# Performance work log

Hardware: AMD Instinct MI355X
Metric: run time of the kernel (lower is better)

The kernel has to match this reference:

```python
import jax, jax.numpy as jnp
import numpy as np

MAX_LENGTH = 10
SOS = 0
H = 1024
V = 32000
B = 256
S = 64


def setup_inputs() -> dict:
    key = jax.random.key(0)
    ks = jax.random.split(key, 16)
    sc = 1.0 / np.sqrt(H)
    return {
        "encoder_outputs": jax.random.normal(ks[0], (B, S, H), jnp.float32),
        "encoder_hidden": jax.random.normal(ks[1], (1, B, H), jnp.float32),
        "target_tensor": jax.random.randint(ks[2], (B, MAX_LENGTH), 0, V),
        "embedding": jax.random.normal(ks[3], (V, H), jnp.float32),
        "Wa_w": jax.random.uniform(ks[4], (H, H), jnp.float32, -sc, sc),
        "Wa_b": jax.random.uniform(ks[5], (H,), jnp.float32, -sc, sc),
        "Ua_w": jax.random.uniform(ks[6], (H, H), jnp.float32, -sc, sc),
        "Ua_b": jax.random.uniform(ks[7], (H,), jnp.float32, -sc, sc),
        "Va_w": jax.random.uniform(ks[8], (1, H), jnp.float32, -sc, sc),
        "Va_b": jax.random.uniform(ks[9], (1,), jnp.float32, -sc, sc),
        "gru_w_ih": jax.random.uniform(ks[10], (3 * H, 2 * H), jnp.float32, -sc, sc),
        "gru_w_hh": jax.random.uniform(ks[11], (3 * H, H), jnp.float32, -sc, sc),
        "gru_b_ih": jax.random.uniform(ks[12], (3 * H,), jnp.float32, -sc, sc),
        "gru_b_hh": jax.random.uniform(ks[13], (3 * H,), jnp.float32, -sc, sc),
        "out_w": jax.random.uniform(ks[14], (V, H), jnp.float32, -sc, sc),
        "out_b": jax.random.uniform(ks[15], (V,), jnp.float32, -sc, sc),
    }


def reference(encoder_outputs, encoder_hidden, target_tensor, embedding,
              Wa_w, Wa_b, Ua_w, Ua_b, Va_w, Va_b,
              gru_w_ih, gru_w_hh, gru_b_ih, gru_b_hh, out_w, out_b):
    keys = encoder_outputs                      # [B,S,H]
    # Ua(keys) is step-invariant: hoist out of the decode loop.
    Uk = jnp.einsum('bsh,kh->bsk', keys, Ua_w) + Ua_b  # [B,S,H]
    h0 = encoder_hidden[0]                      # [B,H]
    # teacher forcing: input at step i is SOS for i=0 else target[:, i-1]
    toks = jnp.concatenate(
        [jnp.full((B, 1), SOS, dtype=target_tensor.dtype),
         target_tensor[:, :MAX_LENGTH - 1]], axis=1).T  # [T,B]

    def step(h, tok):
        emb = embedding[tok]                               # [B,H] (dropout = identity in eval)
        wq = jnp.dot(h, Wa_w.T) + Wa_b                     # [B,H]
        e = jnp.tanh(wq[:, None, :] + Uk)                  # [B,S,H]
        scores = jnp.einsum('bsh,h->bs', e, Va_w[0]) + Va_b[0]
        w = jax.nn.softmax(scores, axis=-1)                # [B,S]
        ctx = jnp.einsum('bs,bsh->bh', w, keys)            # [B,H]
        x = jnp.concatenate([emb, ctx], axis=-1)           # [B,2H]
        gi = jnp.dot(x, gru_w_ih.T) + gru_b_ih             # [B,3H]
        gh = jnp.dot(h, gru_w_hh.T) + gru_b_hh             # [B,3H]
        ir, iz, inn = jnp.split(gi, 3, axis=-1)
        hr, hz, hn = jnp.split(gh, 3, axis=-1)
        r = jax.nn.sigmoid(ir + hr)
        z = jax.nn.sigmoid(iz + hz)
        n = jnp.tanh(inn + r * hn)
        h2 = (1.0 - z) * n + z * h                         # [B,H]
        logits = jnp.dot(h2, out_w.T) + out_b              # [B,V]
        return h2, (logits, w)

    h_last, (logits, attn) = jax.lax.scan(step, h0, toks)
    dec_out = jax.nn.log_softmax(jnp.transpose(logits, (1, 0, 2)), axis=-1)  # [B,T,V]
    attentions = jnp.transpose(attn, (1, 0, 2))            # [B,T,S]
    return dec_out, h_last[None, :, :], attentions
```

## Files before the change

kernel.cpp:

```cpp
#include <hip/hip_runtime.h>
#include <math.h>

#define H 1024
#define V 32000
#define B 256
#define S 64
#define T 10

#define GBK 32

typedef __attribute__((ext_vector_type(8))) short bf16x8;
typedef __attribute__((ext_vector_type(4))) float f32x4;

static __device__ __forceinline__ unsigned short f2bf(float f) {
  unsigned int u = __float_as_uint(f);
  u += 0x7fff + ((u >> 16) & 1);
  return (unsigned short)(u >> 16);
}
static __device__ __forceinline__ float bf2f(unsigned short u) {
  return __uint_as_float(((unsigned int)u) << 16);
}
static __device__ __forceinline__ float fast_tanh(float x) {
  float e = __expf(2.f * x);
  return 1.f - 2.f * __builtin_amdgcn_rcpf(e + 1.f);
}
static __device__ __forceinline__ float fast_sigmoid(float x) {
  return __builtin_amdgcn_rcpf(1.f + __expf(-x));
}

static __device__ __forceinline__ void load_lds16(const void* g, void* l) {
  __builtin_amdgcn_global_load_lds(
      (const __attribute__((address_space(1))) unsigned int*)g,
      (__attribute__((address_space(3))) unsigned int*)l, 16, 0, 0);
}

static __device__ __forceinline__ int lds_off(int row, int g) {
  return row * GBK + ((g ^ ((row >> 1) & 3)) * 8);
}

template <int TM, int TN, int MODE>
__global__ __launch_bounds__(256) void gemm_mfma(
    const unsigned short* __restrict__ A, const unsigned short* __restrict__ W,
    const float* __restrict__ aux, float* __restrict__ C,
    unsigned short* __restrict__ Cb, float* __restrict__ partials,
    int M, int N, int K, int ldc, int pstride) {
  constexpr int FM = (TM == 128) ? 4 : 2;
  constexpr int FN = (TN == 128) ? 4 : 2;
  constexpr int CA = TM / 64;
  constexpr int CB = TN / 64;
  constexpr int LOADS = CA + CB;

  __shared__ unsigned short lsA[3][TM * GBK];
  __shared__ unsigned short lsB[3][TN * GBK];
  const int tid = threadIdx.x;
  const int lane = tid & 63;
  const int w = tid >> 6;
  const int mBase = blockIdx.y * TM;
  const int nBase = blockIdx.x * TN;
  const int rowBase = (w >> 1) * (TM / 2);
  const int colBase = (w & 1) * (TN / 2);

  const int fr = lane & 15;
  const int fkU = lane >> 4;
  const int fg = lane >> 4;

  f32x4 acc[FM][FN] = {};

  auto STAGE = [&](int buf, int k0) {
#pragma unroll
    for (int i = 0; i < CA; ++i) {
      int chunk = i * 256 + tid;
      int row = chunk >> 2;
      int u = chunk & 3;
      int col = (u ^ ((row >> 1) & 3)) * 8;
      load_lds16(A + (size_t)(mBase + row) * K + k0 + col,
                 &lsA[buf][chunk * 8]);
    }
#pragma unroll
    for (int i = 0; i < CB; ++i) {
      int chunk = i * 256 + tid;
      int row = chunk >> 2;
      int u = chunk & 3;
      int col = (u ^ ((row >> 1) & 3)) * 8;
      load_lds16(W + (size_t)(nBase + row) * K + k0 + col,
                 &lsB[buf][chunk * 8]);
    }
  };

  const int NT = K / GBK;
  STAGE(0, 0);
  STAGE(1, GBK);
  int cb = 0;
  for (int t = 0; t < NT; ++t) {
    if (t + 1 < NT) {
      asm volatile("s_waitcnt vmcnt(%0)\n\ts_barrier" :: "i"(LOADS) : "memory");
    } else {
      asm volatile("s_waitcnt vmcnt(0)\n\ts_barrier" ::: "memory");
    }
    if (t + 2 < NT) STAGE((cb + 2) % 3, (t + 2) * GBK);

    bf16x8 af[FM], bfr[FN];
#pragma unroll
    for (int m = 0; m < FM; ++m)
      af[m] = *(const bf16x8*)&lsA[cb][lds_off(rowBase + m * 16 + fr, fkU)];
#pragma unroll
    for (int n = 0; n < FN; ++n)
      bfr[n] = *(const bf16x8*)&lsB[cb][lds_off(colBase + n * 16 + fr, fkU)];
#pragma unroll
    for (int m = 0; m < FM; ++m)
#pragma unroll
      for (int n = 0; n < FN; ++n)
        acc[m][n] = __builtin_amdgcn_mfma_f32_16x16x32_bf16(
            af[m], bfr[n], acc[m][n], 0, 0, 0);
    cb = (cb + 1) % 3;
  }

#pragma unroll
  for (int m = 0; m < FM; ++m) {
    int colg[FN];
    float bv[FN];
#pragma unroll
    for (int n = 0; n < FN; ++n) {
      colg[n] = nBase + colBase + n * 16 + fr;
      if constexpr (MODE != 2) bv[n] = aux[colg[n]];
    }
#pragma unroll
    for (int r = 0; r < 4; ++r) {
      const int rowg = mBase + rowBase + m * 16 + fg * 4 + r;
      float v[FN];
#pragma unroll
      for (int n = 0; n < FN; ++n) {
        if constexpr (MODE == 2)
          v[n] = acc[m][n][r] + aux[(size_t)rowg * ldc + colg[n]];
        else
          v[n] = acc[m][n][r] + bv[n];
        if constexpr (MODE == 1 || MODE == 3)
          Cb[(size_t)rowg * ldc + colg[n]] = f2bf(v[n]);
        else
          C[(size_t)rowg * ldc + colg[n]] = v[n];
      }
      if constexpr (MODE == 3) {
        float mx = fmaxf(fmaxf(v[0], v[1]), fmaxf(v[2], v[3]));
        mx = fmaxf(mx, __shfl_xor(mx, 1, 64));
        mx = fmaxf(mx, __shfl_xor(mx, 2, 64));
        mx = fmaxf(mx, __shfl_xor(mx, 4, 64));
        mx = fmaxf(mx, __shfl_xor(mx, 8, 64));
        float se = __expf(v[0] - mx) + __expf(v[1] - mx) +
                   __expf(v[2] - mx) + __expf(v[3] - mx);
        se += __shfl_xor(se, 1, 64);
        se += __shfl_xor(se, 2, 64);
        se += __shfl_xor(se, 4, 64);
        se += __shfl_xor(se, 8, 64);
        if (fr == 0) {
          float2* pp = (float2*)partials;
          pp[(size_t)rowg * pstride + blockIdx.x * 2 + (w & 1)] =
              make_float2(mx, se);
        }
      }
    }
  }
}

__global__ __launch_bounds__(256) void cvt_bf16_kernel(
    const float* __restrict__ src, unsigned short* __restrict__ dst) {
  size_t i = ((size_t)blockIdx.x * 256 + threadIdx.x) * 8;
  float4 a = *(const float4*)&src[i];
  float4 b = *(const float4*)&src[i + 4];
  ushort4 lo, hi;
  lo.x = f2bf(a.x); lo.y = f2bf(a.y); lo.z = f2bf(a.z); lo.w = f2bf(a.w);
  hi.x = f2bf(b.x); hi.y = f2bf(b.y); hi.z = f2bf(b.z); hi.w = f2bf(b.w);
  *(ushort4*)&dst[i] = lo;
  *(ushort4*)&dst[i + 4] = hi;
}

__global__ __launch_bounds__(256) void cvt_split_wih(
    const float* __restrict__ w_ih, unsigned short* __restrict__ Wemb,
    unsigned short* __restrict__ Wctx) {
  size_t base = ((size_t)blockIdx.x * 256 + threadIdx.x) * 8;
  int row = (int)(base >> 11);
  int col = (int)(base & 2047);
  float4 a = *(const float4*)&w_ih[base];
  float4 b = *(const float4*)&w_ih[base + 4];
  ushort4 lo, hi;
  lo.x = f2bf(a.x); lo.y = f2bf(a.y); lo.z = f2bf(a.z); lo.w = f2bf(a.w);
  hi.x = f2bf(b.x); hi.y = f2bf(b.y); hi.z = f2bf(b.z); hi.w = f2bf(b.w);
  unsigned short* dst = (col < H) ? (Wemb + (size_t)row * H + col)
                                  : (Wctx + (size_t)row * H + col - H);
  *(ushort4*)dst = lo;
  *(ushort4*)(dst + 4) = hi;
}

__global__ __launch_bounds__(256) void build_fused_bias(
    const float* __restrict__ Wa_b, const float* __restrict__ b_hh,
    float* __restrict__ fb) {
  int i = blockIdx.x * 256 + threadIdx.x;
  fb[i] = (i < H) ? Wa_b[i] : b_hh[i - H];
}

__global__ __launch_bounds__(256) void embed_all_kernel(
    const int* __restrict__ target, const float* __restrict__ emb,
    unsigned short* __restrict__ embAll) {
  int idx = blockIdx.x * 256 + threadIdx.x;
  int h8 = (idx & 127) * 8;
  int tb = idx >> 7;
  int t = tb >> 8;
  int b = tb & 255;
  int tok = (t == 0) ? 0 : target[b * T + (t - 1)];
  const float* e = emb + (size_t)tok * H + h8;
  float4 a = *(const float4*)e;
  float4 c = *(const float4*)(e + 4);
  ushort4 lo, hi;
  lo.x = f2bf(a.x); lo.y = f2bf(a.y); lo.z = f2bf(a.z); lo.w = f2bf(a.w);
  hi.x = f2bf(c.x); hi.y = f2bf(c.y); hi.z = f2bf(c.z); hi.w = f2bf(c.w);
  unsigned short* d = embAll + (size_t)tb * H + h8;
  *(ushort4*)d = lo;
  *(ushort4*)(d + 4) = hi;
}

__global__ __launch_bounds__(256) void attn_fused_kernel(
    const float* __restrict__ wqgh, const unsigned short* __restrict__ Uk_bf,
    const unsigned short* __restrict__ keys_bf,
    const float* __restrict__ Va_w, const float* __restrict__ Va_b,
    float* __restrict__ out_attn, unsigned short* __restrict__ ctx_bf, int t) {
  const int b = blockIdx.x;
  const int tid = threadIdx.x;
  __shared__ float wqs[H];
  __shared__ float vas[H];
  __shared__ float sw[S];

  ((float4*)wqs)[tid] = ((const float4*)(wqgh + (size_t)b * 4 * H))[tid];
  ((float4*)vas)[tid] = ((const float4*)Va_w)[tid];
  __syncthreads();

  const int s = tid >> 2;
  const int hc = (tid & 3) * 256;
  const unsigned short* uk = Uk_bf + ((size_t)b * S + s) * H + hc;
  float sum = 0.f;
#pragma unroll 4
  for (int i = 0; i < 256; i += 8) {
    bf16x8 u = *(const bf16x8*)&uk[i];
#pragma unroll
    for (int j = 0; j < 8; ++j) {
      float e = fast_tanh(wqs[hc + i + j] + bf2f((unsigned short)u[j]));
      sum += e * vas[hc + i + j];
    }
  }
  sum += __shfl_xor(sum, 1, 64);
  sum += __shfl_xor(sum, 2, 64);
  if ((tid & 3) == 0) sw[s] = sum + Va_b[0];
  __syncthreads();

  if (tid < 64) {
    float v = sw[tid];
    float m = v;
    for (int off = 32; off > 0; off >>= 1) m = fmaxf(m, __shfl_xor(m, off, 64));
    float e = __expf(v - m);
    float sm = e;
    for (int off = 32; off > 0; off >>= 1) sm += __shfl_xor(sm, off, 64);
    float wv = e / sm;
    sw[tid] = wv;
    out_attn[((size_t)b * T + t) * S + tid] = wv;
  }
  __syncthreads();

  const unsigned short* kb = keys_bf + (size_t)b * S * H + tid * 4;
  float c0 = 0.f, c1 = 0.f, c2 = 0.f, c3 = 0.f;
#pragma unroll 8
  for (int s2 = 0; s2 < S; ++s2) {
    float wv = sw[s2];
    ushort4 kv = *(const ushort4*)&kb[(size_t)s2 * H];
    c0 += wv * bf2f(kv.x);
    c1 += wv * bf2f(kv.y);
    c2 += wv * bf2f(kv.z);
    c3 += wv * bf2f(kv.w);
  }
  ushort4 o;
  o.x = f2bf(c0); o.y = f2bf(c1); o.z = f2bf(c2); o.w = f2bf(c3);
  *(ushort4*)&ctx_bf[(size_t)b * H + tid * 4] = o;
}

__global__ __launch_bounds__(256) void gru_kernel(
    const float* __restrict__ gi, const float* __restrict__ wqgh,
    const float* __restrict__ h_in, float* __restrict__ h_out,
    unsigned short* __restrict__ h_out_bf) {
  int idx = blockIdx.x * 256 + threadIdx.x;
  int b = idx >> 10;
  int j = idx & (H - 1);
  const float* gib = gi + (size_t)b * 3 * H;
  const float* ghb = wqgh + (size_t)b * 4 * H + H;
  float r = fast_sigmoid(gib[j] + ghb[j]);
  float z = fast_sigmoid(gib[H + j] + ghb[H + j]);
  float n = fast_tanh(gib[2 * H + j] + r * ghb[2 * H + j]);
  float hp = h_in[idx];
  float ho = (1.f - z) * n + z * hp;
  h_out[idx] = ho;
  h_out_bf[idx] = f2bf(ho);
}

__global__ __launch_bounds__(256) void logsm_reduce_kernel(
    const float* __restrict__ partials, float* __restrict__ ls, int P) {
  const int row = blockIdx.x;
  const int tid = threadIdx.x;
  const float2* pp = (const float2*)partials + (size_t)row * P;
  __shared__ float red[256];
  float mx = -INFINITY;
  for (int i = tid; i < P; i += 256) mx = fmaxf(mx, pp[i].x);
  red[tid] = mx;
  __syncthreads();
  for (int off = 128; off > 0; off >>= 1) {
    if (tid < off) red[tid] = fmaxf(red[tid], red[tid + off]);
    __syncthreads();
  }
  mx = red[0];
  __syncthreads();
  float sm = 0.f;
  for (int i = tid; i < P; i += 256) sm += pp[i].y * __expf(pp[i].x - mx);
  red[tid] = sm;
  __syncthreads();
  for (int off = 128; off > 0; off >>= 1) {
    if (tid < off) red[tid] += red[tid + off];
    __syncthreads();
  }
  if (tid == 0) ls[row] = mx + __logf(red[0]);
}

__global__ __launch_bounds__(256) void logsm_sub_kernel(
    const unsigned short* __restrict__ logits_bf, const float* __restrict__ ls,
    float* __restrict__ dec) {
  const int tb = blockIdx.y;
  const int t = tb >> 8;
  const int b = tb & 255;
  const int i8 = (blockIdx.x * 256 + threadIdx.x) * 8;
  if (i8 < V) {
    float l = ls[tb];
    const unsigned short* src = logits_bf + (size_t)tb * V + i8;
    bf16x8 u = *(const bf16x8*)src;
    float* d = dec + (size_t)b * T * V + (size_t)t * V + i8;
    float4 o0, o1;
    o0.x = bf2f((unsigned short)u[0]) - l; o0.y = bf2f((unsigned short)u[1]) - l;
    o0.z = bf2f((unsigned short)u[2]) - l; o0.w = bf2f((unsigned short)u[3]) - l;
    o1.x = bf2f((unsigned short)u[4]) - l; o1.y = bf2f((unsigned short)u[5]) - l;
    o1.z = bf2f((unsigned short)u[6]) - l; o1.w = bf2f((unsigned short)u[7]) - l;
    *(float4*)d = o0;
    *(float4*)(d + 4) = o1;
  }
}

__global__ __launch_bounds__(256) void copy_kernel(
    const float* __restrict__ src, float* __restrict__ dst, int n) {
  int i = blockIdx.x * 256 + threadIdx.x;
  if (i < n) dst[i] = src[i];
}

extern "C" void kernel_launch(void* const* d_in, const int* in_sizes, int n_in,
                              void* d_out, int out_size, void* d_ws, size_t ws_size,
                              hipStream_t stream) {
  const float* keys       = (const float*)d_in[0];
  const float* enc_hidden = (const float*)d_in[1];
  const int*   target     = (const int*)d_in[2];
  const float* embedding  = (const float*)d_in[3];
  const float* Wa_w = (const float*)d_in[4];
  const float* Wa_b = (const float*)d_in[5];
  const float* Ua_w = (const float*)d_in[6];
  const float* Ua_b = (const float*)d_in[7];
  const float* Va_w = (const float*)d_in[8];
  const float* Va_b = (const float*)d_in[9];
  const float* gru_w_ih = (const float*)d_in[10];
  const float* gru_w_hh = (const float*)d_in[11];
  const float* gru_b_ih = (const float*)d_in[12];
  const float* gru_b_hh = (const float*)d_in[13];
  const float* out_w = (const float*)d_in[14];
  const float* out_b = (const float*)d_in[15];

  float* out = (float*)d_out;
  float* out_dec  = out;
  float* out_h    = out + (size_t)B * T * V;
  float* out_attn = out + (size_t)B * T * V + (size_t)B * H;

  char* p = (char*)d_ws;
  unsigned short* keys_bf = (unsigned short*)p; p += (size_t)B * S * H * 2;
  unsigned short* outw_bf = (unsigned short*)p; p += (size_t)V * H * 2;
  unsigned short* Uaw_bf  = (unsigned short*)p; p += (size_t)H * H * 2;
  unsigned short* fusedW  = (unsigned short*)p; p += (size_t)4 * H * H * 2;
  float*          fusedB  = (float*)p;          p += (size_t)4 * H * 4;
  unsigned short* Wemb_bf = (unsigned short*)p; p += (size_t)3 * H * H * 2;
  unsigned short* Wctx_bf = (unsigned short*)p; p += (size_t)3 * H * H * 2;
  unsigned short* embAll  = (unsigned short*)p; p += (size_t)T * B * H * 2;
  unsigned short* Uk_bf   = (unsigned short*)p; p += (size_t)B * S * H * 2;
  float*          giE     = (float*)p;          p += (size_t)T * B * 3 * H * 4;
  float*          wqgh    = (float*)p;          p += (size_t)B * 4 * H * 4;
  unsigned short* ctx_bf  = (unsigned short*)p; p += (size_t)B * H * 2;
  float*          gi      = (float*)p;          p += (size_t)B * 3 * H * 4;
  float*          hA      = (float*)p;          p += (size_t)B * H * 4;
  float*          hB      = (float*)p;          p += (size_t)B * H * 4;
  unsigned short* hAll    = (unsigned short*)p; p += (size_t)(T + 1) * B * H * 2;
  unsigned short* logits_bf = (unsigned short*)p; p += (size_t)T * B * V * 2;
  float*          parts   = (float*)p;          p += (size_t)T * B * 500 * 2 * 4;
  float*          ls      = (float*)p;          p += (size_t)T * B * 4;

  cvt_bf16_kernel<<<(B * S * H) / 2048, 256, 0, stream>>>(keys, keys_bf);
  cvt_bf16_kernel<<<((size_t)V * H) / 2048, 256, 0, stream>>>(out_w, outw_bf);
  cvt_bf16_kernel<<<(H * H) / 2048, 256, 0, stream>>>(Ua_w, Uaw_bf);
  cvt_bf16_kernel<<<(H * H) / 2048, 256, 0, stream>>>(Wa_w, fusedW);
  cvt_bf16_kernel<<<(3 * H * H) / 2048, 256, 0, stream>>>(gru_w_hh,
                                                          fusedW + (size_t)H * H);
  build_fused_bias<<<(4 * H) / 256, 256, 0, stream>>>(Wa_b, gru_b_hh, fusedB);
  cvt_split_wih<<<(3 * H * 2 * H) / 2048, 256, 0, stream>>>(gru_w_ih, Wemb_bf,
                                                            Wctx_bf);
  embed_all_kernel<<<(T * B * H / 8) / 256, 256, 0, stream>>>(target, embedding,
                                                              embAll);
  cvt_bf16_kernel<<<(B * H) / 2048, 256, 0, stream>>>(enc_hidden, hAll);

  gemm_mfma<128, 128, 1><<<dim3(H / 128, (B * S) / 128), 256, 0, stream>>>(
      keys_bf, Uaw_bf, Ua_b, nullptr, Uk_bf, nullptr, B * S, H, H, H, 0);
  gemm_mfma<128, 128, 0><<<dim3(3 * H / 128, (T * B) / 128), 256, 0, stream>>>(
      embAll, Wemb_bf, gru_b_ih, giE, nullptr, nullptr, T * B, 3 * H, H, 3 * H, 0);

  const float* h_in = enc_hidden;
  float* hbufs[2] = {hA, hB};

  for (int t = 0; t < T; ++t) {
    const unsigned short* hbf_in = hAll + (size_t)t * B * H;
    unsigned short* hbf_out = hAll + (size_t)(t + 1) * B * H;
    float* h_out = hbufs[t & 1];

    gemm_mfma<64, 64, 0><<<dim3(4 * H / 64, B / 64), 256, 0, stream>>>(
        hbf_in, fusedW, fusedB, wqgh, nullptr, nullptr, B, 4 * H, H, 4 * H, 0);
    attn_fused_kernel<<<B, 256, 0, stream>>>(
        wqgh, Uk_bf, keys_bf, Va_w, Va_b, out_attn, ctx_bf, t);
    gemm_mfma<64, 64, 2><<<dim3(3 * H / 64, B / 64), 256, 0, stream>>>(
        ctx_bf, Wctx_bf, giE + (size_t)t * B * 3 * H, gi, nullptr, nullptr,
        B, 3 * H, H, 3 * H, 0);
    gru_kernel<<<(B * H) / 256, 256, 0, stream>>>(gi, wqgh, h_in, h_out, hbf_out);

    h_in = h_out;
  }

  gemm_mfma<128, 128, 3><<<dim3(V / 128, (T * B) / 128), 256, 0, stream>>>(
      hAll + (size_t)B * H, outw_bf, out_b, nullptr, logits_bf, parts,
      T * B, V, H, V, 500);
  logsm_reduce_kernel<<<T * B, 256, 0, stream>>>(parts, ls, 500);
  logsm_sub_kernel<<<dim3((V + 2047) / 2048, T * B), 256, 0, stream>>>(
      logits_bf, ls, out_dec);

  copy_kernel<<<(B * H + 255) / 256, 256, 0, stream>>>(h_in, out_h, B * H);
}
```

Before: 1.042 ms.

## Fuse context GEMM with GRU update and remap GEMM grids per XCD

Replaces the per-step ctx GEMM plus separate GRU elementwise kernel with one kernel that computes the r/z/n gate tiles together and applies the GRU update in its epilogue, removing the gi round-trip through global memory and one launch per step. It also adds an XCD-aware block remapping to the other GEMMs, so that consecutive M tiles sharing a weight tile land on the same XCD and can reuse it from L2. The fused kernel has only 64 blocks per step, which may underfill the GPU.

```diff
diff --git a/kernel.cpp b/kernel.cpp
--- a/kernel.cpp
+++ b/kernel.cpp
@@ -38,7 +38,7 @@
   return row * GBK + ((g ^ ((row >> 1) & 3)) * 8);
 }
 
-template <int TM, int TN, int MODE>
+template <int TM, int TN, int MODE, int GRIDMODE>
 __global__ __launch_bounds__(256) void gemm_mfma(
     const unsigned short* __restrict__ A, const unsigned short* __restrict__ W,
     const float* __restrict__ aux, float* __restrict__ C,
@@ -55,8 +55,23 @@
   const int tid = threadIdx.x;
   const int lane = tid & 63;
   const int w = tid >> 6;
-  const int mBase = blockIdx.y * TM;
-  const int nBase = blockIdx.x * TN;
+
+  int mIdx, nIdx;
+  if constexpr (GRIDMODE == 1) {
+    const int nwg = gridDim.x * gridDim.y;
+    const int orig = blockIdx.y * gridDim.x + blockIdx.x;
+    const int q = nwg >> 3, rr = nwg & 7;
+    const int xcd = orig & 7, rest = orig >> 3;
+    const int wgid =
+        (xcd < rr ? xcd * (q + 1) : rr * (q + 1) + (xcd - rr) * q) + rest;
+    mIdx = wgid % gridDim.x;
+    nIdx = wgid / gridDim.x;
+  } else {
+    mIdx = blockIdx.y;
+    nIdx = blockIdx.x;
+  }
+  const int mBase = mIdx * TM;
+  const int nBase = nIdx * TN;
   const int rowBase = (w >> 1) * (TM / 2);
   const int colBase = (w & 1) * (TN / 2);
 
@@ -153,12 +168,111 @@
         se += __shfl_xor(se, 8, 64);
         if (fr == 0) {
           float2* pp = (float2*)partials;
-          pp[(size_t)rowg * pstride + blockIdx.x * 2 + (w & 1)] =
+          pp[(size_t)rowg * pstride + nIdx * 2 + (w & 1)] =
               make_float2(mx, se);
         }
       }
     }
   }
+}
+
+__global__ __launch_bounds__(256) void gemm_gru_kernel(
+    const unsigned short* __restrict__ A,
+    const unsigned short* __restrict__ W3,
+    const float* __restrict__ giE_t,
+    const float* __restrict__ wqgh,
+    const float* __restrict__ h_in,
+    float* __restrict__ h_out,
+    unsigned short* __restrict__ h_out_bf) {
+  constexpr int LOADS = 4;
+  __shared__ unsigned short lsA[3][64 * GBK];
+  __shared__ unsigned short lsW[3][3][64 * GBK];
+  const int tid = threadIdx.x;
+  const int lane = tid & 63;
+  const int w = tid >> 6;
+
+  const int nwg = gridDim.x * gridDim.y;
+  const int orig = blockIdx.y * gridDim.x + blockIdx.x;
+  const int q = nwg >> 3;
+  const int xcd = orig & 7, rest = orig >> 3;
+  const int wgid = xcd * q + rest;
+  const int mBase = (wgid % gridDim.x) * 64;
+  const int jBase = (wgid / gridDim.x) * 64;
+
+  const int rowBase = (w >> 1) * 32;
+  const int colBase = (w & 1) * 32;
+  const int fr = lane & 15;
+  const int fkU = lane >> 4;
+  const int fg = lane >> 4;
+
+  f32x4 acc[3][2][2] = {};
+
+  auto STAGE = [&](int buf, int k0) {
+    int chunk = tid;
+    int row = chunk >> 2;
+    int u = chunk & 3;
+    int col = (u ^ ((row >> 1) & 3)) * 8;
+    load_lds16(A + (size_t)(mBase + row) * H + k0 + col, &lsA[buf][chunk * 8]);
+#pragma unroll
+    for (int g = 0; g < 3; ++g)
+      load_lds16(W3 + (size_t)(g * H + jBase + row) * H + k0 + col,
+                 &lsW[buf][g][chunk * 8]);
+  };
+
+  const int NT = H / GBK;
+  STAGE(0, 0);
+  STAGE(1, GBK);
+  int cb = 0;
+  for (int t = 0; t < NT; ++t) {
+    if (t + 1 < NT) {
+      asm volatile("s_waitcnt vmcnt(%0)\n\ts_barrier" :: "i"(LOADS) : "memory");
+    } else {
+      asm volatile("s_waitcnt vmcnt(0)\n\ts_barrier" ::: "memory");
+    }
+    if (t + 2 < NT) STAGE((cb + 2) % 3, (t + 2) * GBK);
+
+    bf16x8 af[2], wf[3][2];
+#pragma unroll
+    for (int m = 0; m < 2; ++m)
+      af[m] = *(const bf16x8*)&lsA[cb][lds_off(rowBase + m * 16 + fr, fkU)];
+#pragma unroll
+    for (int g = 0; g < 3; ++g)
+#pragma unroll
+      for (int n = 0; n < 2; ++n)
+        wf[g][n] =
+            *(const bf16x8*)&lsW[cb][g][lds_off(colBase + n * 16 + fr, fkU)];
+#pragma unroll
+    for (int g = 0; g < 3; ++g)
+#pragma unroll
+      for (int m = 0; m < 2; ++m)
+#pragma unroll
+        for (int n = 0; n < 2; ++n)
+          acc[g][m][n] = __builtin_amdgcn_mfma_f32_16x16x32_bf16(
+              af[m], wf[g][n], acc[g][m][n], 0, 0, 0);
+    cb = (cb + 1) % 3;
+  }
+
+#pragma unroll
+  for (int m = 0; m < 2; ++m)
+#pragma unroll
+    for (int n = 0; n < 2; ++n)
+#pragma unroll
+      for (int r = 0; r < 4; ++r) {
+        const int row = mBase + rowBase + m * 16 + fg * 4 + r;
+        const int col = jBase + colBase + n * 16 + fr;
+        const float* giE_row = giE_t + (size_t)row * 3 * H;
+        const float* gh_row = wqgh + (size_t)row * 4 * H + H;
+        float gr = acc[0][m][n][r] + giE_row[col];
+        float gz = acc[1][m][n][r] + giE_row[H + col];
+        float gn = acc[2][m][n][r] + giE_row[2 * H + col];
+        float rr = fast_sigmoid(gr + gh_row[col]);
+        float zz = fast_sigmoid(gz + gh_row[H + col]);
+        float nn = fast_tanh(gn + rr * gh_row[2 * H + col]);
+        float hp = h_in[(size_t)row * H + col];
+        float ho = (1.f - zz) * nn + zz * hp;
+        h_out[(size_t)row * H + col] = ho;
+        h_out_bf[(size_t)row * H + col] = f2bf(ho);
+      }
 }
 
 __global__ __launch_bounds__(256) void cvt_bf16_kernel(
@@ -277,24 +391,6 @@
   ushort4 o;
   o.x = f2bf(c0); o.y = f2bf(c1); o.z = f2bf(c2); o.w = f2bf(c3);
   *(ushort4*)&ctx_bf[(size_t)b * H + tid * 4] = o;
-}
-
-__global__ __launch_bounds__(256) void gru_kernel(
-    const float* __restrict__ gi, const float* __restrict__ wqgh,
-    const float* __restrict__ h_in, float* __restrict__ h_out,
-    unsigned short* __restrict__ h_out_bf) {
-  int idx = blockIdx.x * 256 + threadIdx.x;
-  int b = idx >> 10;
-  int j = idx & (H - 1);
-  const float* gib = gi + (size_t)b * 3 * H;
-  const float* ghb = wqgh + (size_t)b * 4 * H + H;
-  float r = fast_sigmoid(gib[j] + ghb[j]);
-  float z = fast_sigmoid(gib[H + j] + ghb[H + j]);
-  float n = fast_tanh(gib[2 * H + j] + r * ghb[2 * H + j]);
-  float hp = h_in[idx];
-  float ho = (1.f - z) * n + z * hp;
-  h_out[idx] = ho;
-  h_out_bf[idx] = f2bf(ho);
 }
 
 __global__ __launch_bounds__(256) void logsm_reduce_kernel(
@@ -390,7 +486,6 @@
   float*          giE     = (float*)p;          p += (size_t)T * B * 3 * H * 4;
   float*          wqgh    = (float*)p;          p += (size_t)B * 4 * H * 4;
   unsigned short* ctx_bf  = (unsigned short*)p; p += (size_t)B * H * 2;
-  float*          gi      = (float*)p;          p += (size_t)B * 3 * H * 4;
   float*          hA      = (float*)p;          p += (size_t)B * H * 4;
   float*          hB      = (float*)p;          p += (size_t)B * H * 4;
   unsigned short* hAll    = (unsigned short*)p; p += (size_t)(T + 1) * B * H * 2;
@@ -411,9 +506,9 @@
                                                               embAll);
   cvt_bf16_kernel<<<(B * H) / 2048, 256, 0, stream>>>(enc_hidden, hAll);
 
-  gemm_mfma<128, 128, 1><<<dim3(H / 128, (B * S) / 128), 256, 0, stream>>>(
+  gemm_mfma<128, 128, 1, 0><<<dim3(H / 128, (B * S) / 128), 256, 0, stream>>>(
       keys_bf, Uaw_bf, Ua_b, nullptr, Uk_bf, nullptr, B * S, H, H, H, 0);
-  gemm_mfma<128, 128, 0><<<dim3(3 * H / 128, (T * B) / 128), 256, 0, stream>>>(
+  gemm_mfma<128, 128, 0, 1><<<dim3((T * B) / 128, 3 * H / 128), 256, 0, stream>>>(
       embAll, Wemb_bf, gru_b_ih, giE, nullptr, nullptr, T * B, 3 * H, H, 3 * H, 0);
 
   const float* h_in = enc_hidden;
@@ -424,19 +519,18 @@
     unsigned short* hbf_out = hAll + (size_t)(t + 1) * B * H;
     float* h_out = hbufs[t & 1];
 
-    gemm_mfma<64, 64, 0><<<dim3(4 * H / 64, B / 64), 256, 0, stream>>>(
+    gemm_mfma<64, 64, 0, 1><<<dim3(B / 64, 4 * H / 64), 256, 0, stream>>>(
         hbf_in, fusedW, fusedB, wqgh, nullptr, nullptr, B, 4 * H, H, 4 * H, 0);
     attn_fused_kernel<<<B, 256, 0, stream>>>(
         wqgh, Uk_bf, keys_bf, Va_w, Va_b, out_attn, ctx_bf, t);
-    gemm_mfma<64, 64, 2><<<dim3(3 * H / 64, B / 64), 256, 0, stream>>>(
-        ctx_bf, Wctx_bf, giE + (size_t)t * B * 3 * H, gi, nullptr, nullptr,
-        B, 3 * H, H, 3 * H, 0);
-    gru_kernel<<<(B * H) / 256, 256, 0, stream>>>(gi, wqgh, h_in, h_out, hbf_out);
+    gemm_gru_kernel<<<dim3(B / 64, H / 64), 256, 0, stream>>>(
+        ctx_bf, Wctx_bf, giE + (size_t)t * B * 3 * H, wqgh, h_in, h_out,
+        hbf_out);
 
     h_in = h_out;
   }
 
-  gemm_mfma<128, 128, 3><<<dim3(V / 128, (T * B) / 128), 256, 0, stream>>>(
+  gemm_mfma<128, 128, 3, 1><<<dim3((T * B) / 128, V / 128), 256, 0, stream>>>(
       hAll + (size_t)B * H, outw_bf, out_b, nullptr, logits_bf, parts,
       T * B, V, H, V, 500);
   logsm_reduce_kernel<<<T * B, 256, 0, stream>>>(parts, ls, 500);
```

After: 1.083 ms. 1.04x slower.
